# Kernel tuning notes

Hardware: AMD Instinct MI355X
Metric: run time of the kernel (lower is better)

The kernel has to match this reference:

```python
import jax, jax.numpy as jnp
import numpy as np

E4M3_MAX = 448.0
BLOCK = 128


def _quant_dequant(x, block=BLOCK):
    # x: [R, C] -> block-wise fake-quantized [R, C]
    R, C = x.shape
    pad_r = (-R) % block
    pad_c = (-C) % block
    xp = jnp.pad(x, ((0, pad_r), (0, pad_c)))
    Rp, Cp = R + pad_r, C + pad_c
    # [nR, block, nC, block] -> [nR, nC, block, block]
    xb = xp.reshape(Rp // block, block, Cp // block, block).transpose(0, 2, 1, 3)
    amax = jnp.max(jnp.abs(xb), axis=(-1, -2), keepdims=True)
    scale = jnp.maximum(amax / E4M3_MAX, 1e-8)
    xq = jnp.clip(jnp.round(xb / scale), -E4M3_MAX, E4M3_MAX)
    xdq = (xq * scale).transpose(0, 2, 1, 3).reshape(Rp, Cp)
    return xdq[:R, :C]


def setup_inputs() -> dict:
    key = jax.random.key(0)
    k1, k2 = jax.random.split(key)
    B, S, D_in, D_out = 4, 2048, 4096, 4096
    x = jax.random.normal(k1, (B, S, D_in), dtype=jnp.float32)
    weight = jax.random.normal(k2, (D_out, D_in), dtype=jnp.float32)
    bias = jnp.zeros((D_out,), dtype=jnp.float32)
    return {"x": x, "weight": weight, "bias": bias}


def reference(x, weight, bias):
    batch_shape = x.shape[:-1]
    in_features = x.shape[-1]
    x_flat = x.reshape(-1, in_features)
    x_dq = _quant_dequant(x_flat)
    w_dq = _quant_dequant(weight)
    out = x_dq @ w_dq.T + bias  # [N, out_features]
    return out.reshape(*batch_shape, weight.shape[0])
```

## Files before the change

### kernel.cpp

```cpp
#include <hip/hip_runtime.h>
#include <hip/hip_fp16.h>
#include <stdint.h>

typedef _Float16 half_t;
typedef half_t half8 __attribute__((ext_vector_type(8)));
typedef float f32x4 __attribute__((ext_vector_type(4)));

#define E4M3_MAX 448.0f
#define MFMA16 __builtin_amdgcn_mfma_f32_16x16x32_f16

constexpr int Mdim = 8192, Ndim = 4096, Kdim = 4096;
constexpr int NKT = Kdim / 64;
constexpr int NITER = NKT / 2;
constexpr int NKB = Kdim / 128;
constexpr int NTN = Ndim / 256;
constexpr int NTM = Mdim / 256;
constexpr int LDS_BYTES = 131072 + 8 * 32 * 4;

__global__ __launch_bounds__(256) void quant_kernel(const float* __restrict__ in,
                                                    half_t* __restrict__ outq,
                                                    float* __restrict__ scales,
                                                    int C) {
    const int cb = blockIdx.x, rb = blockIdx.y;
    const int tid = threadIdx.x;
    const int col4 = tid & 31;
    const int rsub = tid >> 5;

    const float* base = in + (size_t)(rb * 128 + rsub) * C + cb * 128 + col4 * 4;

    f32x4 v[16];
    float amax = 0.0f;
#pragma unroll
    for (int p = 0; p < 16; ++p) {
        v[p] = *(const f32x4*)(base + (size_t)p * 8 * C);
        amax = fmaxf(amax, fmaxf(fmaxf(fabsf(v[p].x), fabsf(v[p].y)),
                                 fmaxf(fabsf(v[p].z), fabsf(v[p].w))));
    }
#pragma unroll
    for (int off = 32; off > 0; off >>= 1)
        amax = fmaxf(amax, __shfl_xor(amax, off, 64));
    __shared__ float red[4];
    if ((tid & 63) == 0) red[tid >> 6] = amax;
    __syncthreads();
    amax = fmaxf(fmaxf(red[0], red[1]), fmaxf(red[2], red[3]));

    const float scale = fmaxf(amax / E4M3_MAX, 1e-8f);
    const float rs = 1.0f / scale;

    half_t* obase = outq + (size_t)(rb * 128 + rsub) * C + cb * 128 + col4 * 4;
#pragma unroll
    for (int p = 0; p < 16; ++p) {
        float q0 = fminf(fmaxf(rintf(v[p].x * rs), -E4M3_MAX), E4M3_MAX);
        float q1 = fminf(fmaxf(rintf(v[p].y * rs), -E4M3_MAX), E4M3_MAX);
        float q2 = fminf(fmaxf(rintf(v[p].z * rs), -E4M3_MAX), E4M3_MAX);
        float q3 = fminf(fmaxf(rintf(v[p].w * rs), -E4M3_MAX), E4M3_MAX);
        union { half_t h[4]; uint64_t u; } pk;
        pk.h[0] = (half_t)q0; pk.h[1] = (half_t)q1;
        pk.h[2] = (half_t)q2; pk.h[3] = (half_t)q3;
        *(uint64_t*)(obase + (size_t)p * 8 * C) = pk.u;
    }
    if (tid == 0) scales[(size_t)rb * gridDim.x + cb] = scale;
}

__device__ __forceinline__ void async16(const half_t* g, char* l) {
    __builtin_amdgcn_global_load_lds((const __attribute__((address_space(1))) void*)g,
                                     (__attribute__((address_space(3))) void*)l, 16, 0, 0);
}

extern __shared__ char smem[];

__global__ __launch_bounds__(512, 2) void gemm_kernel(
    const half_t* __restrict__ A, const half_t* __restrict__ B,
    const float* __restrict__ sA, const float* __restrict__ sB,
    const float* __restrict__ bias, float* __restrict__ C) {

    const int tid = threadIdx.x;
    const int lane = tid & 63;
    const int wid = tid >> 6;
    const int lo = lane & 15, hi = lane >> 4;
    const int wr = wid >> 2;
    const int wc = wid & 3;

    const int bid = blockIdx.x;
    constexpr int cpx = (NTM * NTN) / 8;
    const int id = (bid & 7) * cpx + (bid >> 3);
    const int tm = id / NTN, tn = id % NTN;

    const int ib = tm * 2 + wr;
    const int jb = tn * 2 + (wc >> 1);
    {
        const int k = lane & 31;
        float s = sA[ib * NKB + k] * sB[jb * NKB + k];
        *(float*)(smem + 131072 + wid * 128 + k * 4) = s;
    }
    __builtin_amdgcn_sched_barrier(0);

    const int r0 = tid >> 3;
    const int ks = ((tid & 7) ^ (r0 & 7)) * 8;
    const half_t* Abase = A + (size_t)(tm * 256 + r0) * Kdim + ks;
    const half_t* Bbase = B + (size_t)(tn * 256 + r0) * Kdim + ks;
    char* ldst = smem + tid * 16;

#define STG_A(b, h, kt) do {                                                              \
    async16(Abase + (size_t)((h) * 128) * Kdim + (kt) * 64,                               \
            ldst + (b) * 32768 + (h) * 16384);                                            \
    async16(Abase + (size_t)((h) * 128 + 64) * Kdim + (kt) * 64,                          \
            ldst + (b) * 32768 + (h) * 16384 + 8192); } while (0)
#define STG_B(b, h, kt) do {                                                              \
    async16(Bbase + (size_t)((h) * 128) * Kdim + (kt) * 64,                               \
            ldst + 65536 + (b) * 32768 + (h) * 16384);                                    \
    async16(Bbase + (size_t)((h) * 128 + 64) * Kdim + (kt) * 64,                          \
            ldst + 65536 + (b) * 32768 + (h) * 16384 + 8192); } while (0)

    STG_B(0, 0, 0); STG_B(0, 1, 0); STG_A(0, 0, 0); STG_A(0, 1, 0);
    STG_B(1, 0, 1); STG_B(1, 1, 1);
    asm volatile("s_waitcnt vmcnt(4)" ::: "memory");
    __builtin_amdgcn_sched_barrier(0);
    __builtin_amdgcn_s_barrier();
    __builtin_amdgcn_sched_barrier(0);

    const int aoff0 = lo * 128 + ((hi ^ (lo & 3)) << 4) + (((lo >> 2) & 1) << 6);
    const int aoff1 = aoff0 ^ 64;
    const char* pA0 = smem + wr * 16384 + aoff0;
    const char* pA1 = smem + wr * 16384 + aoff1;
    const char* pB0 = smem + 65536 + (wc >> 1) * 16384 + (wc & 1) * 8192 + aoff0;
    const char* pB1 = smem + 65536 + (wc >> 1) * 16384 + (wc & 1) * 8192 + aoff1;

    f32x4 acc[8][4] = {};
    half8 bfr[4][2];

#define BARSEQ                                                                            \
    __builtin_amdgcn_sched_barrier(0);                                                    \
    __builtin_amdgcn_s_barrier();                                                         \
    __builtin_amdgcn_sched_barrier(0);

#define LDA4(b, q, A00, A01, A10, A11)                                                    \
    half8 A00 = *(const half8*)(pA0 + (b) * 32768 + (2 * (q)) * 2048);                    \
    half8 A01 = *(const half8*)(pA1 + (b) * 32768 + (2 * (q)) * 2048);                    \
    half8 A10 = *(const half8*)(pA0 + (b) * 32768 + (2 * (q) + 1) * 2048);                \
    half8 A11 = *(const half8*)(pA1 + (b) * 32768 + (2 * (q) + 1) * 2048);

#define MFMAQ(q, A00, A01, A10, A11)                                                      \
    __builtin_amdgcn_s_setprio(1);                                                        \
    acc[2*(q)][0]   = MFMA16(A00, bfr[0][0], acc[2*(q)][0],   0, 0, 0);                   \
    acc[2*(q)][1]   = MFMA16(A00, bfr[1][0], acc[2*(q)][1],   0, 0, 0);                   \
    acc[2*(q)][2]   = MFMA16(A00, bfr[2][0], acc[2*(q)][2],   0, 0, 0);                   \
    acc[2*(q)][3]   = MFMA16(A00, bfr[3][0], acc[2*(q)][3],   0, 0, 0);                   \
    acc[2*(q)+1][0] = MFMA16(A10, bfr[0][0], acc[2*(q)+1][0], 0, 0, 0);                   \
    acc[2*(q)+1][1] = MFMA16(A10, bfr[1][0], acc[2*(q)+1][1], 0, 0, 0);                   \
    acc[2*(q)+1][2] = MFMA16(A10, bfr[2][0], acc[2*(q)+1][2], 0, 0, 0);                   \
    acc[2*(q)+1][3] = MFMA16(A10, bfr[3][0], acc[2*(q)+1][3], 0, 0, 0);                   \
    acc[2*(q)][0]   = MFMA16(A01, bfr[0][1], acc[2*(q)][0],   0, 0, 0);                   \
    acc[2*(q)][1]   = MFMA16(A01, bfr[1][1], acc[2*(q)][1],   0, 0, 0);                   \
    acc[2*(q)][2]   = MFMA16(A01, bfr[2][1], acc[2*(q)][2],   0, 0, 0);                   \
    acc[2*(q)][3]   = MFMA16(A01, bfr[3][1], acc[2*(q)][3],   0, 0, 0);                   \
    acc[2*(q)+1][0] = MFMA16(A11, bfr[0][1], acc[2*(q)+1][0], 0, 0, 0);                   \
    acc[2*(q)+1][1] = MFMA16(A11, bfr[1][1], acc[2*(q)+1][1], 0, 0, 0);                   \
    acc[2*(q)+1][2] = MFMA16(A11, bfr[2][1], acc[2*(q)+1][2], 0, 0, 0);                   \
    acc[2*(q)+1][3] = MFMA16(A11, bfr[3][1], acc[2*(q)+1][3], 0, 0, 0);                   \
    __builtin_amdgcn_s_setprio(0);

    for (int i = 0; i < NITER; ++i) {
        const int kta1 = 2 * i + 1;
        const int ktb0 = (2 * i + 2) & (NKT - 1);
        const int ktb1 = (2 * i + 3) & (NKT - 1);

        const float s = *(const float*)(smem + 131072 + wid * 128 + i * 4);
        const half_t sh = (half_t)s;
        const half8 s8 = {sh, sh, sh, sh, sh, sh, sh, sh};

        {
            half8 l00 = *(const half8*)(pB0 + 0 * 2048), l01 = *(const half8*)(pB1 + 0 * 2048);
            half8 l10 = *(const half8*)(pB0 + 1 * 2048), l11 = *(const half8*)(pB1 + 1 * 2048);
            half8 l20 = *(const half8*)(pB0 + 2 * 2048), l21 = *(const half8*)(pB1 + 2 * 2048);
            half8 l30 = *(const half8*)(pB0 + 3 * 2048), l31 = *(const half8*)(pB1 + 3 * 2048);
            LDA4(0, 0, a00, a01, a10, a11)
            BARSEQ
            bfr[0][0] = l00 * s8; bfr[0][1] = l01 * s8;
            bfr[1][0] = l10 * s8; bfr[1][1] = l11 * s8;
            bfr[2][0] = l20 * s8; bfr[2][1] = l21 * s8;
            bfr[3][0] = l30 * s8; bfr[3][1] = l31 * s8;
            MFMAQ(0, a00, a01, a10, a11)
        }
        {
            LDA4(0, 1, a00, a01, a10, a11)
            STG_A(1, 0, kta1);
            BARSEQ
            MFMAQ(1, a00, a01, a10, a11)
        }
        {
            LDA4(0, 2, a00, a01, a10, a11)
            STG_B(0, 0, ktb0); STG_A(1, 1, kta1);
            BARSEQ
            MFMAQ(2, a00, a01, a10, a11)
        }
        {
            LDA4(0, 3, a00, a01, a10, a11)
            STG_B(0, 1, ktb0);
            asm volatile("s_waitcnt vmcnt(2)" ::: "memory");
            BARSEQ
            MFMAQ(3, a00, a01, a10, a11)
        }
        {
            half8 l00 = *(const half8*)(pB0 + 32768 + 0 * 2048), l01 = *(const half8*)(pB1 + 32768 + 0 * 2048);
            half8 l10 = *(const half8*)(pB0 + 32768 + 1 * 2048), l11 = *(const half8*)(pB1 + 32768 + 1 * 2048);
            half8 l20 = *(const half8*)(pB0 + 32768 + 2 * 2048), l21 = *(const half8*)(pB1 + 32768 + 2 * 2048);
            half8 l30 = *(const half8*)(pB0 + 32768 + 3 * 2048), l31 = *(const half8*)(pB1 + 32768 + 3 * 2048);
            LDA4(1, 0, a00, a01, a10, a11)
            BARSEQ
            bfr[0][0] = l00 * s8; bfr[0][1] = l01 * s8;
            bfr[1][0] = l10 * s8; bfr[1][1] = l11 * s8;
            bfr[2][0] = l20 * s8; bfr[2][1] = l21 * s8;
            bfr[3][0] = l30 * s8; bfr[3][1] = l31 * s8;
            MFMAQ(0, a00, a01, a10, a11)
        }
        {
            LDA4(1, 1, a00, a01, a10, a11)
            STG_A(0, 0, ktb0); STG_A(0, 1, ktb0);
            BARSEQ
            MFMAQ(1, a00, a01, a10, a11)
        }
        {
            LDA4(1, 2, a00, a01, a10, a11)
            STG_B(1, 0, ktb1);
            BARSEQ
            MFMAQ(2, a00, a01, a10, a11)
        }
        {
            LDA4(1, 3, a00, a01, a10, a11)
            STG_B(1, 1, ktb1);
            asm volatile("s_waitcnt vmcnt(4)" ::: "memory");
            BARSEQ
            MFMAQ(3, a00, a01, a10, a11)
        }
    }

    const int rbase = tm * 256 + wr * 128;
    const int cbase = tn * 256 + wc * 64;
    float bv0 = bias[cbase + 0 * 16 + lo];
    float bv1 = bias[cbase + 1 * 16 + lo];
    float bv2 = bias[cbase + 2 * 16 + lo];
    float bv3 = bias[cbase + 3 * 16 + lo];
#pragma unroll
    for (int m = 0; m < 8; ++m) {
        const int r0r = rbase + m * 16 + hi * 4;
#pragma unroll
        for (int r = 0; r < 4; ++r) {
            float* crow = C + (size_t)(r0r + r) * Ndim + cbase + lo;
            crow[0]  = acc[m][0][r] + bv0;
            crow[16] = acc[m][1][r] + bv1;
            crow[32] = acc[m][2][r] + bv2;
            crow[48] = acc[m][3][r] + bv3;
        }
    }
}

extern "C" void kernel_launch(void* const* d_in, const int* in_sizes, int n_in,
                              void* d_out, int out_size, void* d_ws, size_t ws_size,
                              hipStream_t stream) {
    const float* x = (const float*)d_in[0];
    const float* w = (const float*)d_in[1];
    const float* bias = (const float*)d_in[2];
    float* out = (float*)d_out;

    if (in_sizes[2] != Ndim || in_sizes[1] != Ndim * Kdim || in_sizes[0] != Mdim * Kdim)
        return;

    const size_t xq_bytes = (size_t)Mdim * Kdim * sizeof(half_t);
    const size_t wq_bytes = (size_t)Ndim * Kdim * sizeof(half_t);
    const size_t sA_bytes = (size_t)(Mdim / 128) * NKB * sizeof(float);
    const size_t sB_bytes = (size_t)(Ndim / 128) * NKB * sizeof(float);
    if (ws_size < xq_bytes + wq_bytes + sA_bytes + sB_bytes) return;

    half_t* xq = (half_t*)d_ws;
    half_t* wq = (half_t*)((char*)d_ws + xq_bytes);
    float* sxa = (float*)((char*)d_ws + xq_bytes + wq_bytes);
    float* swb = (float*)((char*)d_ws + xq_bytes + wq_bytes + sA_bytes);

    quant_kernel<<<dim3(Kdim / 128, Mdim / 128), 256, 0, stream>>>(x, xq, sxa, Kdim);
    quant_kernel<<<dim3(Kdim / 128, Ndim / 128), 256, 0, stream>>>(w, wq, swb, Kdim);

    (void)hipFuncSetAttribute((const void*)gemm_kernel,
                              hipFuncAttributeMaxDynamicSharedMemorySize, LDS_BYTES);

    gemm_kernel<<<dim3(NTM * NTN), dim3(512), LDS_BYTES, stream>>>(xq, wq, sxa, swb, bias, out);
}
```

Before: 285.1 us.

## Reorder A-tile staging so each quarter step refills only already-consumed LDS slices

Changes the A-tile LDS layout and staging so A is loaded as four 64-row slices, with each quarter step issuing loads for slices whose region has already been read. A-tile prefetch for the next buffer now starts earlier and is spread evenly across the first two sub-steps, and the vmcnt waits are rebalanced. It also defers the per-iteration scale load into the fold step and adds a final vmcnt(0) drain. The aim is to overlap global-to-LDS traffic better with MFMA work, at the risk of hazards from the new buffer-reuse ordering.

```diff
diff --git a/kernel.cpp b/kernel.cpp
--- a/kernel.cpp
+++ b/kernel.cpp
@@ -99,32 +99,31 @@
     const int ks = ((tid & 7) ^ (r0 & 7)) * 8;
     const half_t* Abase = A + (size_t)(tm * 256 + r0) * Kdim + ks;
     const half_t* Bbase = B + (size_t)(tn * 256 + r0) * Kdim + ks;
-    char* ldst = smem + tid * 16;
-
-#define STG_A(b, h, kt) do {                                                              \
-    async16(Abase + (size_t)((h) * 128) * Kdim + (kt) * 64,                               \
-            ldst + (b) * 32768 + (h) * 16384);                                            \
-    async16(Abase + (size_t)((h) * 128 + 64) * Kdim + (kt) * 64,                          \
-            ldst + (b) * 32768 + (h) * 16384 + 8192); } while (0)
+    char* ldstA = smem + tid * 16;
+    char* ldstB = smem + 65536 + tid * 16;
+
+#define STG_AS(b, s, kt)                                                                  \
+    async16(Abase + (size_t)((s) * 64) * Kdim + (kt) * 64,                                \
+            ldstA + (b) * 32768 + (s) * 8192)
 #define STG_B(b, h, kt) do {                                                              \
     async16(Bbase + (size_t)((h) * 128) * Kdim + (kt) * 64,                               \
-            ldst + 65536 + (b) * 32768 + (h) * 16384);                                    \
+            ldstB + (b) * 32768 + (h) * 16384);                                           \
     async16(Bbase + (size_t)((h) * 128 + 64) * Kdim + (kt) * 64,                          \
-            ldst + 65536 + (b) * 32768 + (h) * 16384 + 8192); } while (0)
-
-    STG_B(0, 0, 0); STG_B(0, 1, 0); STG_A(0, 0, 0); STG_A(0, 1, 0);
+            ldstB + (b) * 32768 + (h) * 16384 + 8192); } while (0)
+
+    STG_B(0, 0, 0); STG_B(0, 1, 0);
+    STG_AS(0, 0, 0); STG_AS(0, 1, 0); STG_AS(0, 2, 0); STG_AS(0, 3, 0);
     STG_B(1, 0, 1); STG_B(1, 1, 1);
     asm volatile("s_waitcnt vmcnt(4)" ::: "memory");
     __builtin_amdgcn_sched_barrier(0);
     __builtin_amdgcn_s_barrier();
     __builtin_amdgcn_sched_barrier(0);
 
-    const int aoff0 = lo * 128 + ((hi ^ (lo & 3)) << 4) + (((lo >> 2) & 1) << 6);
-    const int aoff1 = aoff0 ^ 64;
-    const char* pA0 = smem + wr * 16384 + aoff0;
-    const char* pA1 = smem + wr * 16384 + aoff1;
-    const char* pB0 = smem + 65536 + (wc >> 1) * 16384 + (wc & 1) * 8192 + aoff0;
-    const char* pB1 = smem + 65536 + (wc >> 1) * 16384 + (wc & 1) * 8192 + aoff1;
+    const int koff0 = ((hi ^ (lo & 3)) << 4) + (((lo >> 2) & 1) << 6);
+    const char* pA0 = smem + wr * 16384 + lo * 128 + koff0;
+    const char* pA1 = smem + wr * 16384 + lo * 128 + (koff0 ^ 64);
+    const char* pB0 = smem + 65536 + wc * 8192 + lo * 128 + koff0;
+    const char* pB1 = smem + 65536 + wc * 8192 + lo * 128 + (koff0 ^ 64);
 
     f32x4 acc[8][4] = {};
     half8 bfr[4][2];
@@ -135,10 +134,10 @@
     __builtin_amdgcn_sched_barrier(0);
 
 #define LDA4(b, q, A00, A01, A10, A11)                                                    \
-    half8 A00 = *(const half8*)(pA0 + (b) * 32768 + (2 * (q)) * 2048);                    \
-    half8 A01 = *(const half8*)(pA1 + (b) * 32768 + (2 * (q)) * 2048);                    \
-    half8 A10 = *(const half8*)(pA0 + (b) * 32768 + (2 * (q) + 1) * 2048);                \
-    half8 A11 = *(const half8*)(pA1 + (b) * 32768 + (2 * (q) + 1) * 2048);
+    half8 A00 = *(const half8*)(pA0 + (b) * 32768 + (q) * 4096);                          \
+    half8 A01 = *(const half8*)(pA1 + (b) * 32768 + (q) * 4096);                          \
+    half8 A10 = *(const half8*)(pA0 + (b) * 32768 + (q) * 4096 + 2048);                   \
+    half8 A11 = *(const half8*)(pA1 + (b) * 32768 + (q) * 4096 + 2048);
 
 #define MFMAQ(q, A00, A01, A10, A11)                                                      \
     __builtin_amdgcn_s_setprio(1);                                                        \
@@ -160,80 +159,89 @@
     acc[2*(q)+1][3] = MFMA16(A11, bfr[3][1], acc[2*(q)+1][3], 0, 0, 0);                   \
     __builtin_amdgcn_s_setprio(0);
 
+#define LDB8(b)                                                                           \
+    half8 bl00 = *(const half8*)(pB0 + (b) * 32768 + 0 * 2048);                           \
+    half8 bl01 = *(const half8*)(pB1 + (b) * 32768 + 0 * 2048);                           \
+    half8 bl10 = *(const half8*)(pB0 + (b) * 32768 + 1 * 2048);                           \
+    half8 bl11 = *(const half8*)(pB1 + (b) * 32768 + 1 * 2048);                           \
+    half8 bl20 = *(const half8*)(pB0 + (b) * 32768 + 2 * 2048);                           \
+    half8 bl21 = *(const half8*)(pB1 + (b) * 32768 + 2 * 2048);                           \
+    half8 bl30 = *(const half8*)(pB0 + (b) * 32768 + 3 * 2048);                           \
+    half8 bl31 = *(const half8*)(pB1 + (b) * 32768 + 3 * 2048);
+
+#define BFOLD                                                                             \
+    {                                                                                     \
+        const float s_ = *(const float*)(smem + 131072 + wid * 128 + i * 4);              \
+        const half_t sh_ = (half_t)s_;                                                    \
+        const half8 s8_ = {sh_, sh_, sh_, sh_, sh_, sh_, sh_, sh_};                       \
+        bfr[0][0] = bl00 * s8_; bfr[0][1] = bl01 * s8_;                                   \
+        bfr[1][0] = bl10 * s8_; bfr[1][1] = bl11 * s8_;                                   \
+        bfr[2][0] = bl20 * s8_; bfr[2][1] = bl21 * s8_;                                   \
+        bfr[3][0] = bl30 * s8_; bfr[3][1] = bl31 * s8_;                                   \
+    }
+
     for (int i = 0; i < NITER; ++i) {
-        const int kta1 = 2 * i + 1;
-        const int ktb0 = (2 * i + 2) & (NKT - 1);
-        const int ktb1 = (2 * i + 3) & (NKT - 1);
-
-        const float s = *(const float*)(smem + 131072 + wid * 128 + i * 4);
-        const half_t sh = (half_t)s;
-        const half8 s8 = {sh, sh, sh, sh, sh, sh, sh, sh};
-
-        {
-            half8 l00 = *(const half8*)(pB0 + 0 * 2048), l01 = *(const half8*)(pB1 + 0 * 2048);
-            half8 l10 = *(const half8*)(pB0 + 1 * 2048), l11 = *(const half8*)(pB1 + 1 * 2048);
-            half8 l20 = *(const half8*)(pB0 + 2 * 2048), l21 = *(const half8*)(pB1 + 2 * 2048);
-            half8 l30 = *(const half8*)(pB0 + 3 * 2048), l31 = *(const half8*)(pB1 + 3 * 2048);
+        const int kA1  = 2 * i + 1;
+        const int ktn0 = (2 * i + 2) & (NKT - 1);
+        const int ktn1 = (2 * i + 3) & (NKT - 1);
+
+        {
+            LDB8(0)
             LDA4(0, 0, a00, a01, a10, a11)
-            BARSEQ
-            bfr[0][0] = l00 * s8; bfr[0][1] = l01 * s8;
-            bfr[1][0] = l10 * s8; bfr[1][1] = l11 * s8;
-            bfr[2][0] = l20 * s8; bfr[2][1] = l21 * s8;
-            bfr[3][0] = l30 * s8; bfr[3][1] = l31 * s8;
+            STG_AS(1, 0, kA1); STG_AS(1, 2, kA1);
+            BARSEQ
+            BFOLD
             MFMAQ(0, a00, a01, a10, a11)
         }
         {
             LDA4(0, 1, a00, a01, a10, a11)
-            STG_A(1, 0, kta1);
+            STG_AS(1, 1, kA1); STG_AS(1, 3, kA1);
             BARSEQ
             MFMAQ(1, a00, a01, a10, a11)
         }
         {
             LDA4(0, 2, a00, a01, a10, a11)
-            STG_B(0, 0, ktb0); STG_A(1, 1, kta1);
+            STG_B(0, 0, ktn0);
             BARSEQ
             MFMAQ(2, a00, a01, a10, a11)
         }
         {
             LDA4(0, 3, a00, a01, a10, a11)
-            STG_B(0, 1, ktb0);
-            asm volatile("s_waitcnt vmcnt(2)" ::: "memory");
+            STG_B(0, 1, ktn0);
+            asm volatile("s_waitcnt vmcnt(4)" ::: "memory");
             BARSEQ
             MFMAQ(3, a00, a01, a10, a11)
         }
         {
-            half8 l00 = *(const half8*)(pB0 + 32768 + 0 * 2048), l01 = *(const half8*)(pB1 + 32768 + 0 * 2048);
-            half8 l10 = *(const half8*)(pB0 + 32768 + 1 * 2048), l11 = *(const half8*)(pB1 + 32768 + 1 * 2048);
-            half8 l20 = *(const half8*)(pB0 + 32768 + 2 * 2048), l21 = *(const half8*)(pB1 + 32768 + 2 * 2048);
-            half8 l30 = *(const half8*)(pB0 + 32768 + 3 * 2048), l31 = *(const half8*)(pB1 + 32768 + 3 * 2048);
+            LDB8(1)
             LDA4(1, 0, a00, a01, a10, a11)
-            BARSEQ
-            bfr[0][0] = l00 * s8; bfr[0][1] = l01 * s8;
-            bfr[1][0] = l10 * s8; bfr[1][1] = l11 * s8;
-            bfr[2][0] = l20 * s8; bfr[2][1] = l21 * s8;
-            bfr[3][0] = l30 * s8; bfr[3][1] = l31 * s8;
+            STG_AS(0, 0, ktn0); STG_AS(0, 2, ktn0);
+            BARSEQ
+            BFOLD
             MFMAQ(0, a00, a01, a10, a11)
         }
         {
             LDA4(1, 1, a00, a01, a10, a11)
-            STG_A(0, 0, ktb0); STG_A(0, 1, ktb0);
+            STG_AS(0, 1, ktn0); STG_AS(0, 3, ktn0);
             BARSEQ
             MFMAQ(1, a00, a01, a10, a11)
         }
         {
             LDA4(1, 2, a00, a01, a10, a11)
-            STG_B(1, 0, ktb1);
+            STG_B(1, 0, ktn1);
             BARSEQ
             MFMAQ(2, a00, a01, a10, a11)
         }
         {
             LDA4(1, 3, a00, a01, a10, a11)
-            STG_B(1, 1, ktb1);
+            STG_B(1, 1, ktn1);
             asm volatile("s_waitcnt vmcnt(4)" ::: "memory");
             BARSEQ
             MFMAQ(3, a00, a01, a10, a11)
         }
     }
+
+    asm volatile("s_waitcnt vmcnt(0)" ::: "memory");
 
     const int rbase = tm * 256 + wr * 128;
     const int cbase = tn * 256 + wc * 64;
```

After: 278.0 us. -2.5%, faster.
